# Optimization experiments

Measured on AMD Instinct MI355X. Metric: run time of the kernel, lower is better.

## Reference

```python
import jax, jax.numpy as jnp
import numpy as np

B, H, W, C, F = 32, 32, 32, 256, 64
K_NEIGH = 32  # L1 pixel-distance cutoff used for the static mask


def _distance_mask(h, w, k):
    # coords: [hw, 2] of (y, x); L1 pixel distances, normalized by max(h, w)
    ys, xs = jnp.meshgrid(jnp.arange(h), jnp.arange(w), indexing='ij')
    coords = jnp.stack([ys, xs], axis=-1).reshape(-1, 2).astype(jnp.float32)
    diff = jnp.abs(coords[:, None, :] - coords[None, :, :]).sum(-1)  # [hw, hw], == cdist p=1
    dist = diff / float(max(h, w))
    return jnp.where(diff <= k, dist, 0.0)


def setup_inputs() -> dict:
    key = jax.random.key(0)
    ks = jax.random.split(key, 7)
    return {
        'feature_map': jax.random.normal(ks[0], (B, H, W, C), dtype=jnp.float32),
        'emb_W': jax.random.normal(ks[1], (F, C), dtype=jnp.float32) * (1.0 / np.sqrt(C)),
        'emb_b': jax.random.normal(ks[2], (F,), dtype=jnp.float32) * 0.01,
        'attn_W': jax.random.normal(ks[3], (C, C), dtype=jnp.float32) * (1.0 / np.sqrt(C)),
        'attn_b': jax.random.normal(ks[4], (C,), dtype=jnp.float32) * 0.01,
        'thr_W': jax.random.normal(ks[5], (1, C), dtype=jnp.float32) * (1.0 / np.sqrt(C)),
        'thr_b': jax.random.normal(ks[6], (1,), dtype=jnp.float32) * 0.01,
        'layer': 0,
    }


def reference(feature_map, emb_W, emb_b, attn_W, attn_b, thr_W, thr_b, layer):
    b, h, w, c = feature_map.shape
    hw = h * w
    x = feature_map.reshape(b, hw, c)  # row-major (y, x) flatten, matches torch view

    # 1x1 conv -> per-pixel linear: instance embeddings [b, hw, F]
    emb = jnp.einsum('bnc,fc->bnf', x, emb_W) + emb_b

    # squared Euclidean pairwise distances (cdist p=2, then squared)
    sq = jnp.sum(emb * emb, axis=-1)  # [b, hw]
    d2 = jnp.maximum(sq[:, :, None] + sq[:, None, :]
                     - 2.0 * jnp.einsum('bnf,bmf->bnm', emb, emb), 0.0)

    mask = _distance_mask(h, w, K_NEIGH)  # [hw, hw] static buffer
    sim = jax.nn.softmax(jnp.exp(-d2) - (1.0 - mask), axis=-1)  # [b, hw, hw]

    # shortcut = attention_conv(feature_map): [b, hw, c]
    shortcut = jnp.einsum('bnc,dc->bnd', x, attn_W) + attn_b

    # per-pixel learned threshold: [b, hw]
    Tinst = (jnp.einsum('bnc,oc->bno', shortcut, thr_W) + thr_b)[..., 0]

    A = jax.nn.softmax(jnp.maximum(sim - Tinst[:, None, :], 0.0), axis=-1)

    # bmm: out[b, i, c] = sum_j shortcut[b, j, c] * A[b, i, j]
    attn_out = jnp.einsum('bjc,bij->bic', shortcut, A)

    res = (x + attn_out).reshape(b, h, w, c)
    return res
```

## Files before the change

### kernel.cpp

```cpp
#include <hip/hip_runtime.h>
#include <hip/hip_bf16.h>


typedef short bf16x8 __attribute__((ext_vector_type(8)));
typedef float f32x4 __attribute__((ext_vector_type(4)));

__device__ __forceinline__ unsigned short f2bf(float f) {
  unsigned u = __float_as_uint(f);
  u += 0x7fffu + ((u >> 16) & 1u);
  return (unsigned short)(u >> 16);
}
__device__ __forceinline__ float bf2f(unsigned short h) {
  return __uint_as_float(((unsigned)h) << 16);
}
__device__ __forceinline__ f32x4 mfma16(bf16x8 a, bf16x8 b, f32x4 c) {
  return __builtin_amdgcn_mfma_f32_16x16x32_bf16(a, b, c, 0, 0, 0);
}
__device__ __forceinline__ int iabs(int v) { return v < 0 ? -v : v; }
__device__ __forceinline__ void load_lds16(const void* g, void* l) {
  __builtin_amdgcn_global_load_lds(
      (const __attribute__((address_space(1))) unsigned int*)g,
      (__attribute__((address_space(3))) unsigned int*)l, 16, 0, 0);
}

__global__ __launch_bounds__(256) void k_prep(const float* __restrict__ x,
                                              const float* __restrict__ embW,
                                              const float* __restrict__ attnW,
                                              unsigned short* __restrict__ xb,
                                              unsigned short* __restrict__ Wb,
                                              unsigned short* __restrict__ Msk63) {
  const int tid = blockIdx.x * 256 + threadIdx.x;
  {
    float4 v = *(const float4*)(x + (size_t)tid * 4);
    ushort4 p; p.x = f2bf(v.x); p.y = f2bf(v.y); p.z = f2bf(v.z); p.w = f2bf(v.w);
    *(ushort4*)(xb + (size_t)tid * 4) = p;
  }
  if (tid < 81920) {
    float v = (tid < 16384) ? embW[tid] : attnW[tid - 16384];
    Wb[tid] = f2bf(v);
  }
  if (tid < 3969) {
    int dy = tid / 63 - 31, dx = tid % 63 - 31;
    int diff = iabs(dy) + iabs(dx);
    float m = (diff <= 32) ? (float)diff * (1.f / 32.f) : 0.f;
    Msk63[tid] = f2bf(__expf(m - 1.f));
  }
}

__global__ __launch_bounds__(256) void k_emb(const unsigned short* __restrict__ xb,
                                             const unsigned short* __restrict__ Wb,
                                             const float* __restrict__ embB,
                                             unsigned short* __restrict__ embb,
                                             float* __restrict__ sq) {
  __shared__ unsigned short xs[64][40];
  __shared__ unsigned short ws[64][40];
  __shared__ float sqls[64];
  const int t = threadIdx.x;
  const int Mbase = blockIdx.x * 64;
  const int lane = t & 63, wave = t >> 6;
  const int wm = wave >> 1, wn = wave & 1;
  const int l15 = lane & 15, quad = lane >> 4;

  f32x4 acc[2][2] = {};
  for (int k0 = 0; k0 < 256; k0 += 32) {
    {
      int row = t >> 2, c0 = (t & 3) * 8;
      *(uint4*)&xs[row][c0] =
          *(const uint4*)(xb + (size_t)(Mbase + row) * 256 + k0 + c0);
    }
    if (t < 64) {
      const unsigned short* wsrc = Wb + (size_t)t * 256 + k0;
      for (int s = 0; s < 4; s++)
        *(uint4*)&ws[t][s * 8] = *(const uint4*)(wsrc + s * 8);
    }
    __syncthreads();
    bf16x8 af[2], bfr[2];
    for (int rt = 0; rt < 2; rt++)
      af[rt] = *(const bf16x8*)&xs[wm * 32 + rt * 16 + l15][quad * 8];
    for (int ct = 0; ct < 2; ct++)
      bfr[ct] = *(const bf16x8*)&ws[wn * 32 + ct * 16 + l15][quad * 8];
    for (int rt = 0; rt < 2; rt++)
      for (int ct = 0; ct < 2; ct++)
        acc[rt][ct] = mfma16(af[rt], bfr[ct], acc[rt][ct]);
    __syncthreads();
  }

  if (t < 64) sqls[t] = 0.f;
  __syncthreads();
  float sp[2][4] = {};
  for (int rt = 0; rt < 2; rt++)
    for (int ct = 0; ct < 2; ct++) {
      int f = wn * 32 + ct * 16 + l15;
      float bias = embB[f];
      for (int r = 0; r < 4; r++) {
        float v = acc[rt][ct][r] + bias;
        unsigned short hb = f2bf(v);
        int rowl = wm * 32 + rt * 16 + quad * 4 + r;
        embb[(size_t)(Mbase + rowl) * 64 + f] = hb;
        float vf = bf2f(hb);
        sp[rt][r] += vf * vf;
      }
    }
  for (int m = 8; m >= 1; m >>= 1)
    for (int rt = 0; rt < 2; rt++)
      for (int r = 0; r < 4; r++)
        sp[rt][r] += __shfl_xor(sp[rt][r], m);
  if (l15 == 0)
    for (int rt = 0; rt < 2; rt++)
      for (int r = 0; r < 4; r++)
        atomicAdd(&sqls[wm * 32 + rt * 16 + quad * 4 + r], sp[rt][r]);
  __syncthreads();
  if (t < 64) sq[Mbase + t] = sqls[t];
}

__global__ __launch_bounds__(256) void k_shortcut(const unsigned short* __restrict__ xb,
                                                  const unsigned short* __restrict__ WbA,
                                                  const float* __restrict__ attnB,
                                                  const float* __restrict__ thrW,
                                                  const float* __restrict__ thrB,
                                                  unsigned short* __restrict__ scT,
                                                  float* __restrict__ Tout) {
  __shared__ unsigned short xs[64][40];
  __shared__ unsigned short ws[256][40];
  __shared__ unsigned short St[256][72];
  const int t = threadIdx.x;
  const int Mbase = blockIdx.x * 64;
  const int lane = t & 63, wave = t >> 6;
  const int wm = wave >> 1, wn = wave & 1;
  const int l15 = lane & 15, quad = lane >> 4;

  f32x4 acc[2][8] = {};
  for (int k0 = 0; k0 < 256; k0 += 32) {
    {
      int row = t >> 2, c0 = (t & 3) * 8;
      *(uint4*)&xs[row][c0] =
          *(const uint4*)(xb + (size_t)(Mbase + row) * 256 + k0 + c0);
    }
    {
      const unsigned short* wsrc = WbA + (size_t)t * 256 + k0;
      for (int s = 0; s < 4; s++)
        *(uint4*)&ws[t][s * 8] = *(const uint4*)(wsrc + s * 8);
    }
    __syncthreads();
    bf16x8 af[2];
    for (int rt = 0; rt < 2; rt++)
      af[rt] = *(const bf16x8*)&xs[wm * 32 + rt * 16 + l15][quad * 8];
    for (int nt = 0; nt < 8; nt++) {
      bf16x8 bfr = *(const bf16x8*)&ws[wn * 128 + nt * 16 + l15][quad * 8];
      for (int rt = 0; rt < 2; rt++)
        acc[rt][nt] = mfma16(af[rt], bfr, acc[rt][nt]);
    }
    __syncthreads();
  }

  for (int rt = 0; rt < 2; rt++)
    for (int nt = 0; nt < 8; nt++) {
      int c = wn * 128 + nt * 16 + l15;
      float bias = attnB[c];
      for (int r = 0; r < 4; r++) {
        float v = acc[rt][nt][r] + bias;
        int j = wm * 32 + rt * 16 + quad * 4 + r;
        St[c][j] = f2bf(v);
      }
    }
  __syncthreads();
  const int b = Mbase >> 10, jbase = Mbase & 1023;
  {
    unsigned short* dst = scT + ((size_t)b * 256 + t) * 1024 + jbase;
    for (int s = 0; s < 8; s++)
      *(uint4*)(dst + s * 8) = *(const uint4*)&St[t][s * 8];
  }
  {
    float tp = 0.f;
    int j = t >> 2, cs = (t & 3) * 64;
    for (int c = 0; c < 64; c++)
      tp += bf2f(St[cs + c][j]) * thrW[cs + c];
    tp += __shfl_xor(tp, 1);
    tp += __shfl_xor(tp, 2);
    if ((t & 3) == 0) Tout[Mbase + j] = tp + thrB[0];
  }
}

__global__ __launch_bounds__(256) void k_scores(const unsigned short* __restrict__ embb,
                                                const float* __restrict__ sq,
                                                const float* __restrict__ T,
                                                const unsigned short* __restrict__ Msk63,
                                                unsigned short* __restrict__ U,
                                                float* __restrict__ Z) {
  __shared__ unsigned short E_lds[16 * 1040];
  __shared__ float rbuf[16];
  const int t = threadIdx.x, lane = t & 63, wave = t >> 6;
  const int b = blockIdx.x >> 6, rb = (blockIdx.x & 63) * 16;
  const int l15 = lane & 15, quad = lane >> 4;
  const unsigned short* eb = embb + (size_t)b * 1024 * 64;

  if (t < 16) rbuf[t] = 0.f;

  const int rowA = rb + l15;
  bf16x8 a0 = *(const bf16x8*)(eb + (size_t)rowA * 64 + quad * 8);
  bf16x8 a1 = *(const bf16x8*)(eb + (size_t)rowA * 64 + 32 + quad * 8);
  const int rloc = quad * 4;
  float nsqi[4]; int yi[4], xi[4];
  for (int r = 0; r < 4; r++) {
    int rowg = rb + rloc + r;
    nsqi[r] = -sq[b * 1024 + rowg];
    yi[r] = rowg >> 5; xi[r] = rowg & 31;
  }
  const int jq = wave * 256;
  float rp[4] = {0.f, 0.f, 0.f, 0.f};
  for (int j0 = jq; j0 < jq + 256; j0 += 16) {
    const int jr = j0 + l15;
    bf16x8 b0 = *(const bf16x8*)(eb + (size_t)jr * 64 + quad * 8);
    bf16x8 b1 = *(const bf16x8*)(eb + (size_t)jr * 64 + 32 + quad * 8);
    f32x4 g = {0.f, 0.f, 0.f, 0.f};
    g = mfma16(a0, b0, g);
    g = mfma16(a1, b1, g);
    float sqj = sq[b * 1024 + jr];
    int yj = jr >> 5, xj = jr & 31;
    for (int r = 0; r < 4; r++) {
      float w = fminf(fmaf(2.f, g[r], nsqi[r] - sqj), 0.f);
      float v = __expf(w);
      int idx = (yi[r] - yj) * 63 + (xi[r] - xj) + 1984;
      float e = __expf(v) * bf2f(Msk63[idx]);
      unsigned short h = f2bf(e);
      E_lds[(rloc + r) * 1040 + jr] = h;
      rp[r] += bf2f(h);
    }
  }
  for (int m = 8; m >= 1; m >>= 1)
    for (int r = 0; r < 4; r++)
      rp[r] += __shfl_xor(rp[r], m);
  __syncthreads();
  if (l15 == 0)
    for (int r = 0; r < 4; r++)
      atomicAdd(&rbuf[rloc + r], rp[r]);
  __syncthreads();

  const int prow = t >> 4, seg = t & 15;
  const float invR = 1.f / rbuf[prow];
  const float* Tb = T + b * 1024;
  unsigned short* ur = U + ((size_t)(b * 1024 + rb + prow)) * 1024;
  float z = 0.f;
  for (int c = 0; c < 8; c++) {
    int j = c * 128 + seg * 8;
    union { bf16x8 v; unsigned short s[8]; } ev;
    ev.v = *(const bf16x8*)&E_lds[prow * 1040 + j];
    float4 t0 = *(const float4*)(Tb + j);
    float4 t1 = *(const float4*)(Tb + j + 4);
    float tf[8] = {t0.x, t0.y, t0.z, t0.w, t1.x, t1.y, t1.z, t1.w};
    union { uint4 v; unsigned short s[8]; } uo;
    for (int k = 0; k < 8; k++) {
      float u = __expf(fmaxf(fmaf(bf2f(ev.s[k]), invR, -tf[k]), 0.f));
      unsigned short h = f2bf(u);
      uo.s[k] = h;
      z += bf2f(h);
    }
    *(uint4*)(ur + j) = uo.v;
  }
  z += __shfl_xor(z, 1);
  z += __shfl_xor(z, 2);
  z += __shfl_xor(z, 4);
  z += __shfl_xor(z, 8);
  if (seg == 0) Z[b * 1024 + rb + prow] = z;
}

__global__ __launch_bounds__(256) void k_out(const unsigned short* __restrict__ U,
                                             const float* __restrict__ Z,
                                             const unsigned short* __restrict__ scT,
                                             const float* __restrict__ x,
                                             float* __restrict__ out) {
  __shared__ unsigned short Ab[128 * 32];
  __shared__ unsigned short Bb[128 * 32];
  const int t = threadIdx.x, lane = t & 63, wave = t >> 6;
  const int wm = wave >> 1, wn = wave & 1;
  const int l15 = lane & 15, quad = lane >> 4;
  const int x8 = blockIdx.x & 7, s = blockIdx.x >> 3;
  const int b = x8 * 4 + (s >> 4), tile = s & 15;
  const int rb = (tile >> 1) * 128, cb = (tile & 1) * 128;

  const unsigned short* Ubase = U + (size_t)b * 1024 * 1024 + (size_t)rb * 1024;
  const unsigned short* Sbase = scT + (size_t)b * 256 * 1024 + (size_t)cb * 1024;

  int c0 = wave * 64 + lane;
  int c1 = c0 + 256;
  const int r0 = c0 >> 2, o0 = (c0 & 3) * 8;
  const int r1 = c1 >> 2, o1 = (c1 & 3) * 8;

  f32x4 acc[4][4] = {};
  for (int j0 = 0; j0 < 1024; j0 += 32) {
    load_lds16(Ubase + (size_t)r0 * 1024 + j0 + o0, Ab + c0 * 8);
    load_lds16(Ubase + (size_t)r1 * 1024 + j0 + o1, Ab + c1 * 8);
    load_lds16(Sbase + (size_t)r0 * 1024 + j0 + o0, Bb + c0 * 8);
    load_lds16(Sbase + (size_t)r1 * 1024 + j0 + o1, Bb + c1 * 8);
    __syncthreads();
    bf16x8 af[4], bf[4];
    for (int i = 0; i < 4; i++)
      af[i] = *(const bf16x8*)&Ab[(wm * 64 + i * 16 + l15) * 32 + quad * 8];
    for (int i = 0; i < 4; i++)
      bf[i] = *(const bf16x8*)&Bb[(wn * 64 + i * 16 + l15) * 32 + quad * 8];
    for (int i = 0; i < 4; i++)
      for (int j = 0; j < 4; j++)
        acc[i][j] = mfma16(af[i], bf[j], acc[i][j]);
    __syncthreads();
  }

  const int colb = cb + wn * 64;
  for (int i = 0; i < 4; i++) {
    int rowb = rb + wm * 64 + i * 16 + quad * 4;
    float iz[4];
    for (int r = 0; r < 4; r++) iz[r] = 1.f / Z[b * 1024 + rowb + r];
    for (int j = 0; j < 4; j++) {
      int c = colb + j * 16 + l15;
      for (int r = 0; r < 4; r++) {
        size_t idx = ((size_t)(b * 1024 + rowb + r)) * 256 + c;
        out[idx] = x[idx] + acc[i][j][r] * iz[r];
      }
    }
  }
}

extern "C" void kernel_launch(void* const* d_in, const int* in_sizes, int n_in,
                              void* d_out, int out_size, void* d_ws, size_t ws_size,
                              hipStream_t stream) {
  const float* x     = (const float*)d_in[0];
  const float* embW  = (const float*)d_in[1];
  const float* embB  = (const float*)d_in[2];
  const float* attnW = (const float*)d_in[3];
  const float* attnB = (const float*)d_in[4];
  const float* thrW  = (const float*)d_in[5];
  const float* thrB  = (const float*)d_in[6];
  float* out = (float*)d_out;

  char* ws = (char*)d_ws;
  unsigned short* embb = (unsigned short*)(ws);
  unsigned short* scT  = (unsigned short*)(ws + (4ull << 20));
  unsigned short* U    = (unsigned short*)(ws + (20ull << 20));
  unsigned short* xb   = (unsigned short*)(ws + (20ull << 20));
  unsigned short* Wb   = (unsigned short*)(ws + (36ull << 20));
  float* sq = (float*)(ws + (84ull << 20));
  float* T  = (float*)(ws + (84ull << 20) + (128ull << 10));
  float* Z  = (float*)(ws + (84ull << 20) + (256ull << 10));
  unsigned short* Msk63 = (unsigned short*)(ws + (84ull << 20) + (384ull << 10));

  k_prep<<<8192, 256, 0, stream>>>(x, embW, attnW, xb, Wb, Msk63);
  k_emb<<<512, 256, 0, stream>>>(xb, Wb, embB, embb, sq);
  k_shortcut<<<512, 256, 0, stream>>>(xb, Wb + 16384, attnB, thrW, thrB, scT, T);
  k_scores<<<2048, 256, 0, stream>>>(embb, sq, T, Msk63, U, Z);
  k_out<<<512, 256, 0, stream>>>(U, Z, scT, x, out);
}
```

Before: 205.1 us.

## Fuse embedding and shortcut GEMMs into one kernel; compute mask via small LDS table

```diff
diff --git a/kernel.cpp b/kernel.cpp
--- a/kernel.cpp
+++ b/kernel.cpp
@@ -27,8 +27,7 @@
                                               const float* __restrict__ embW,
                                               const float* __restrict__ attnW,
                                               unsigned short* __restrict__ xb,
-                                              unsigned short* __restrict__ Wb,
-                                              unsigned short* __restrict__ Msk63) {
+                                              unsigned short* __restrict__ Wb) {
   const int tid = blockIdx.x * 256 + threadIdx.x;
   {
     float4 v = *(const float4*)(x + (size_t)tid * 4);
@@ -39,142 +38,106 @@
     float v = (tid < 16384) ? embW[tid] : attnW[tid - 16384];
     Wb[tid] = f2bf(v);
   }
-  if (tid < 3969) {
-    int dy = tid / 63 - 31, dx = tid % 63 - 31;
-    int diff = iabs(dy) + iabs(dx);
-    float m = (diff <= 32) ? (float)diff * (1.f / 32.f) : 0.f;
-    Msk63[tid] = f2bf(__expf(m - 1.f));
-  }
-}
-
-__global__ __launch_bounds__(256) void k_emb(const unsigned short* __restrict__ xb,
+}
+
+__global__ __launch_bounds__(256) void k_lin(const unsigned short* __restrict__ xb,
                                              const unsigned short* __restrict__ Wb,
                                              const float* __restrict__ embB,
+                                             const float* __restrict__ attnB,
+                                             const float* __restrict__ thrW,
+                                             const float* __restrict__ thrB,
                                              unsigned short* __restrict__ embb,
-                                             float* __restrict__ sq) {
-  __shared__ unsigned short xs[64][40];
-  __shared__ unsigned short ws[64][40];
-  __shared__ float sqls[64];
+                                             float* __restrict__ sq,
+                                             unsigned short* __restrict__ scT,
+                                             float* __restrict__ Tout) {
+  __shared__ union {
+    struct { unsigned short xs[64][40]; unsigned short ws[320][40]; } a;
+    unsigned short St[256][72];
+  } sm;
   const int t = threadIdx.x;
   const int Mbase = blockIdx.x * 64;
   const int lane = t & 63, wave = t >> 6;
   const int wm = wave >> 1, wn = wave & 1;
   const int l15 = lane & 15, quad = lane >> 4;
 
-  f32x4 acc[2][2] = {};
+  f32x4 acc[2][10] = {};
   for (int k0 = 0; k0 < 256; k0 += 32) {
     {
       int row = t >> 2, c0 = (t & 3) * 8;
-      *(uint4*)&xs[row][c0] =
+      *(uint4*)&sm.a.xs[row][c0] =
           *(const uint4*)(xb + (size_t)(Mbase + row) * 256 + k0 + c0);
     }
-    if (t < 64) {
+    {
       const unsigned short* wsrc = Wb + (size_t)t * 256 + k0;
       for (int s = 0; s < 4; s++)
-        *(uint4*)&ws[t][s * 8] = *(const uint4*)(wsrc + s * 8);
-    }
-    __syncthreads();
-    bf16x8 af[2], bfr[2];
-    for (int rt = 0; rt < 2; rt++)
-      af[rt] = *(const bf16x8*)&xs[wm * 32 + rt * 16 + l15][quad * 8];
-    for (int ct = 0; ct < 2; ct++)
-      bfr[ct] = *(const bf16x8*)&ws[wn * 32 + ct * 16 + l15][quad * 8];
-    for (int rt = 0; rt < 2; rt++)
-      for (int ct = 0; ct < 2; ct++)
-        acc[rt][ct] = mfma16(af[rt], bfr[ct], acc[rt][ct]);
-    __syncthreads();
-  }
-
-  if (t < 64) sqls[t] = 0.f;
-  __syncthreads();
-  float sp[2][4] = {};
-  for (int rt = 0; rt < 2; rt++)
-    for (int ct = 0; ct < 2; ct++) {
-      int f = wn * 32 + ct * 16 + l15;
-      float bias = embB[f];
-      for (int r = 0; r < 4; r++) {
-        float v = acc[rt][ct][r] + bias;
-        unsigned short hb = f2bf(v);
-        int rowl = wm * 32 + rt * 16 + quad * 4 + r;
-        embb[(size_t)(Mbase + rowl) * 64 + f] = hb;
-        float vf = bf2f(hb);
-        sp[rt][r] += vf * vf;
+        *(uint4*)&sm.a.ws[t][s * 8] = *(const uint4*)(wsrc + s * 8);
+      if (t < 64) {
+        const unsigned short* wsrc2 = Wb + (size_t)(256 + t) * 256 + k0;
+        for (int s = 0; s < 4; s++)
+          *(uint4*)&sm.a.ws[256 + t][s * 8] = *(const uint4*)(wsrc2 + s * 8);
       }
-    }
-  for (int m = 8; m >= 1; m >>= 1)
-    for (int rt = 0; rt < 2; rt++)
-      for (int r = 0; r < 4; r++)
-        sp[rt][r] += __shfl_xor(sp[rt][r], m);
-  if (l15 == 0)
-    for (int rt = 0; rt < 2; rt++)
-      for (int r = 0; r < 4; r++)
-        atomicAdd(&sqls[wm * 32 + rt * 16 + quad * 4 + r], sp[rt][r]);
-  __syncthreads();
-  if (t < 64) sq[Mbase + t] = sqls[t];
-}
-
-__global__ __launch_bounds__(256) void k_shortcut(const unsigned short* __restrict__ xb,
-                                                  const unsigned short* __restrict__ WbA,
-                                                  const float* __restrict__ attnB,
-                                                  const float* __restrict__ thrW,
-                                                  const float* __restrict__ thrB,
-                                                  unsigned short* __restrict__ scT,
-                                                  float* __restrict__ Tout) {
-  __shared__ unsigned short xs[64][40];
-  __shared__ unsigned short ws[256][40];
-  __shared__ unsigned short St[256][72];
-  const int t = threadIdx.x;
-  const int Mbase = blockIdx.x * 64;
-  const int lane = t & 63, wave = t >> 6;
-  const int wm = wave >> 1, wn = wave & 1;
-  const int l15 = lane & 15, quad = lane >> 4;
-
-  f32x4 acc[2][8] = {};
-  for (int k0 = 0; k0 < 256; k0 += 32) {
-    {
-      int row = t >> 2, c0 = (t & 3) * 8;
-      *(uint4*)&xs[row][c0] =
-          *(const uint4*)(xb + (size_t)(Mbase + row) * 256 + k0 + c0);
-    }
-    {
-      const unsigned short* wsrc = WbA + (size_t)t * 256 + k0;
-      for (int s = 0; s < 4; s++)
-        *(uint4*)&ws[t][s * 8] = *(const uint4*)(wsrc + s * 8);
     }
     __syncthreads();
     bf16x8 af[2];
+    af[0] = *(const bf16x8*)&sm.a.xs[wm * 32 + l15][quad * 8];
+    af[1] = *(const bf16x8*)&sm.a.xs[wm * 32 + 16 + l15][quad * 8];
+    for (int nt = 0; nt < 10; nt++) {
+      bf16x8 bfr = *(const bf16x8*)&sm.a.ws[wn * 160 + nt * 16 + l15][quad * 8];
+      acc[0][nt] = mfma16(af[0], bfr, acc[0][nt]);
+      acc[1][nt] = mfma16(af[1], bfr, acc[1][nt]);
+    }
+    __syncthreads();
+  }
+
+  if (wn == 0) {
+    float sp[2][4] = {{0.f,0.f,0.f,0.f},{0.f,0.f,0.f,0.f}};
     for (int rt = 0; rt < 2; rt++)
-      af[rt] = *(const bf16x8*)&xs[wm * 32 + rt * 16 + l15][quad * 8];
-    for (int nt = 0; nt < 8; nt++) {
-      bf16x8 bfr = *(const bf16x8*)&ws[wn * 128 + nt * 16 + l15][quad * 8];
+      for (int nt = 0; nt < 4; nt++) {
+        int n = nt * 16 + l15;
+        float bias = embB[n];
+        for (int r = 0; r < 4; r++) {
+          float v = acc[rt][nt][r] + bias;
+          unsigned short hb = f2bf(v);
+          int row = wm * 32 + rt * 16 + quad * 4 + r;
+          embb[(size_t)(Mbase + row) * 64 + n] = hb;
+          float vf = bf2f(hb);
+          sp[rt][r] += vf * vf;
+        }
+      }
+    for (int m = 8; m >= 1; m >>= 1)
       for (int rt = 0; rt < 2; rt++)
-        acc[rt][nt] = mfma16(af[rt], bfr, acc[rt][nt]);
-    }
-    __syncthreads();
+        for (int r = 0; r < 4; r++)
+          sp[rt][r] += __shfl_xor(sp[rt][r], m);
+    if (l15 == 0)
+      for (int rt = 0; rt < 2; rt++)
+        for (int r = 0; r < 4; r++)
+          sq[Mbase + wm * 32 + rt * 16 + quad * 4 + r] = sp[rt][r];
   }
 
   for (int rt = 0; rt < 2; rt++)
-    for (int nt = 0; nt < 8; nt++) {
-      int c = wn * 128 + nt * 16 + l15;
+    for (int nt = 0; nt < 10; nt++) {
+      int n = wn * 160 + nt * 16 + l15;
+      if (n < 64) continue;
+      int c = n - 64;
       float bias = attnB[c];
       for (int r = 0; r < 4; r++) {
         float v = acc[rt][nt][r] + bias;
-        int j = wm * 32 + rt * 16 + quad * 4 + r;
-        St[c][j] = f2bf(v);
+        sm.St[c][wm * 32 + rt * 16 + quad * 4 + r] = f2bf(v);
       }
     }
   __syncthreads();
+
   const int b = Mbase >> 10, jbase = Mbase & 1023;
   {
     unsigned short* dst = scT + ((size_t)b * 256 + t) * 1024 + jbase;
     for (int s = 0; s < 8; s++)
-      *(uint4*)(dst + s * 8) = *(const uint4*)&St[t][s * 8];
+      *(uint4*)(dst + s * 8) = *(const uint4*)&sm.St[t][s * 8];
   }
   {
     float tp = 0.f;
     int j = t >> 2, cs = (t & 3) * 64;
     for (int c = 0; c < 64; c++)
-      tp += bf2f(St[cs + c][j]) * thrW[cs + c];
+      tp += bf2f(sm.St[cs + c][j]) * thrW[cs + c];
     tp += __shfl_xor(tp, 1);
     tp += __shfl_xor(tp, 2);
     if ((t & 3) == 0) Tout[Mbase + j] = tp + thrB[0];
@@ -184,17 +147,22 @@
 __global__ __launch_bounds__(256) void k_scores(const unsigned short* __restrict__ embb,
                                                 const float* __restrict__ sq,
                                                 const float* __restrict__ T,
-                                                const unsigned short* __restrict__ Msk63,
                                                 unsigned short* __restrict__ U,
                                                 float* __restrict__ Z) {
   __shared__ unsigned short E_lds[16 * 1040];
   __shared__ float rbuf[16];
+  __shared__ float mtab[64];
   const int t = threadIdx.x, lane = t & 63, wave = t >> 6;
   const int b = blockIdx.x >> 6, rb = (blockIdx.x & 63) * 16;
   const int l15 = lane & 15, quad = lane >> 4;
   const unsigned short* eb = embb + (size_t)b * 1024 * 64;
 
   if (t < 16) rbuf[t] = 0.f;
+  if (t < 64) {
+    float m = (t <= 32) ? (float)t * (1.f / 32.f) : 0.f;
+    mtab[t] = __expf(m - 1.f);
+  }
+  __syncthreads();
 
   const int rowA = rb + l15;
   bf16x8 a0 = *(const bf16x8*)(eb + (size_t)rowA * 64 + quad * 8);
@@ -220,11 +188,10 @@
     for (int r = 0; r < 4; r++) {
       float w = fminf(fmaf(2.f, g[r], nsqi[r] - sqj), 0.f);
       float v = __expf(w);
-      int idx = (yi[r] - yj) * 63 + (xi[r] - xj) + 1984;
-      float e = __expf(v) * bf2f(Msk63[idx]);
-      unsigned short h = f2bf(e);
-      E_lds[(rloc + r) * 1040 + jr] = h;
-      rp[r] += bf2f(h);
+      int diff = iabs(yi[r] - yj) + iabs(xi[r] - xj);
+      float e = __expf(v) * mtab[diff];
+      E_lds[(rloc + r) * 1040 + jr] = f2bf(e);
+      rp[r] += e;
     }
   }
   for (int m = 8; m >= 1; m >>= 1)
@@ -340,11 +307,9 @@
   float* sq = (float*)(ws + (84ull << 20));
   float* T  = (float*)(ws + (84ull << 20) + (128ull << 10));
   float* Z  = (float*)(ws + (84ull << 20) + (256ull << 10));
-  unsigned short* Msk63 = (unsigned short*)(ws + (84ull << 20) + (384ull << 10));
-
-  k_prep<<<8192, 256, 0, stream>>>(x, embW, attnW, xb, Wb, Msk63);
-  k_emb<<<512, 256, 0, stream>>>(xb, Wb, embB, embb, sq);
-  k_shortcut<<<512, 256, 0, stream>>>(xb, Wb + 16384, attnB, thrW, thrB, scT, T);
-  k_scores<<<2048, 256, 0, stream>>>(embb, sq, T, Msk63, U, Z);
+
+  k_prep<<<8192, 256, 0, stream>>>(x, embW, attnW, xb, Wb);
+  k_lin<<<512, 256, 0, stream>>>(xb, Wb, embB, attnB, thrW, thrB, embb, sq, scT, T);
+  k_scores<<<2048, 256, 0, stream>>>(embb, sq, T, U, Z);
   k_out<<<512, 256, 0, stream>>>(U, Z, scT, x, out);
 }
```

After: 198.8 us. 3.1% less time.
